# Optimization experiments

Hardware: AMD Instinct MI355X
Metric: run time of the kernel (lower is better)

Reference implementation:

```python
import jax, jax.numpy as jnp
import numpy as np

TAU = 1.0   # temperature
BETA = 1.0  # instance_alingment_weight


def setup_inputs() -> dict:
    key = jax.random.key(0)
    k1, k2, k3 = jax.random.split(key, 3)
    N, D = 1024, 128
    return {
        "x": jax.random.normal(k1, (N, D), dtype=jnp.float32),
        "aug_x": jax.random.normal(k2, (N, D), dtype=jnp.float32),
        "label_prompt_embedding": jax.random.normal(k3, (N, D), dtype=jnp.float32),
    }


def _pair_loss(x, y, scale):
    # positive distances: ||x_i - y_i|| / (tau * sqrt(D)), shape [N]
    pos = jnp.linalg.norm(x - y, axis=1) * scale
    # pairwise distance matrix [N, N] via broadcasted [N, N, D] diff (as original)
    dm = jnp.linalg.norm(x[:, None, :] - y[None, :, :], axis=-1) * scale
    denom = jnp.sum(jnp.exp(dm), axis=1)  # [N]
    # log(exp(pos) / denom) == pos - log(denom)
    return jnp.mean(pos - jnp.log(denom))


def reference(x, aug_x, label_prompt_embedding):
    D = x.shape[-1]
    scale = 1.0 / (TAU * np.sqrt(D).astype(np.float32))
    center_alignment_loss = _pair_loss(x, label_prompt_embedding, scale)
    instance_alignment_loss = _pair_loss(x, aug_x, scale)
    alignment_loss = center_alignment_loss + BETA * instance_alignment_loss
    return (alignment_loss, center_alignment_loss, instance_alignment_loss)
```

## Files before the change

kernel.cpp:

```cpp
#include <hip/hip_runtime.h>
#include <math.h>

#define NN 1024
#define DD 128

typedef __bf16 bf16x8 __attribute__((ext_vector_type(8)));
typedef float  floatx4 __attribute__((ext_vector_type(4)));

__global__ __launch_bounds__(256) void align_pair_kernel(
    const float* __restrict__ x,
    const float* __restrict__ y_center,
    const float* __restrict__ y_aug,
    float* __restrict__ partials )
{
    const float SCALE = 0.08838834764831845f;
    const int p    = blockIdx.y;
    const float* __restrict__ y = p ? y_aug : y_center;
    const int i0   = blockIdx.x * 16;
    const int tid  = threadIdx.x;
    const int w    = tid >> 6;
    const int lane = tid & 63;
    const int col  = lane & 15;
    const int quad = lane >> 4;

    const float* xrow = x + (size_t)(i0 + col) * DD + quad * 8;
    bf16x8 afrag[4];
    float nx_own = 0.f;
#pragma unroll
    for (int c = 0; c < 4; ++c) {
        const float4 u0 = *(const float4*)(xrow + c * 32);
        const float4 u1 = *(const float4*)(xrow + c * 32 + 4);
        nx_own += u0.x*u0.x + u0.y*u0.y + u0.z*u0.z + u0.w*u0.w;
        nx_own += u1.x*u1.x + u1.y*u1.y + u1.z*u1.z + u1.w*u1.w;
        bf16x8 f;
        f[0]=(__bf16)u0.x; f[1]=(__bf16)u0.y; f[2]=(__bf16)u0.z; f[3]=(__bf16)u0.w;
        f[4]=(__bf16)u1.x; f[5]=(__bf16)u1.y; f[6]=(__bf16)u1.z; f[7]=(__bf16)u1.w;
        afrag[c] = f;
    }
    nx_own += __shfl_xor(nx_own, 16);
    nx_own += __shfl_xor(nx_own, 32);
    float nxr[4];
#pragma unroll
    for (int r = 0; r < 4; ++r) nxr[r] = __shfl(nx_own, quad * 4 + r);

    float denom[4] = {0.f, 0.f, 0.f, 0.f};
    float pos[4]   = {0.f, 0.f, 0.f, 0.f};

    for (int t = 0; t < 16; ++t) {
        const int j0 = t * 64 + w * 16;
        const float* yrow = y + (size_t)(j0 + col) * DD + quad * 8;
        bf16x8 bfrag[4];
        float ny_own = 0.f;
#pragma unroll
        for (int c = 0; c < 4; ++c) {
            const float4 u0 = *(const float4*)(yrow + c * 32);
            const float4 u1 = *(const float4*)(yrow + c * 32 + 4);
            ny_own += u0.x*u0.x + u0.y*u0.y + u0.z*u0.z + u0.w*u0.w;
            ny_own += u1.x*u1.x + u1.y*u1.y + u1.z*u1.z + u1.w*u1.w;
            bf16x8 f;
            f[0]=(__bf16)u0.x; f[1]=(__bf16)u0.y; f[2]=(__bf16)u0.z; f[3]=(__bf16)u0.w;
            f[4]=(__bf16)u1.x; f[5]=(__bf16)u1.y; f[6]=(__bf16)u1.z; f[7]=(__bf16)u1.w;
            bfrag[c] = f;
        }
        ny_own += __shfl_xor(ny_own, 16);
        ny_own += __shfl_xor(ny_own, 32);

        floatx4 acc = {0.f, 0.f, 0.f, 0.f};
#pragma unroll
        for (int c = 0; c < 4; ++c)
            acc = __builtin_amdgcn_mfma_f32_16x16x32_bf16(afrag[c], bfrag[c], acc, 0, 0, 0);

#pragma unroll
        for (int r = 0; r < 4; ++r) {
            const int row = quad * 4 + r;
            float d2 = fmaf(-2.f, acc[r], nxr[r] + ny_own);
            d2 = fmaxf(d2, 0.f);
            const float dm = SCALE * sqrtf(d2);
            denom[r] += __expf(dm);
            if (j0 + col == i0 + row) pos[r] = dm;
        }
    }

#pragma unroll
    for (int r = 0; r < 4; ++r) {
#pragma unroll
        for (int m = 1; m < 16; m <<= 1) {
            denom[r] += __shfl_xor(denom[r], m);
            pos[r]   += __shfl_xor(pos[r], m);
        }
    }

    __shared__ float ld_den[4][16];
    __shared__ float ld_pos[4][16];
    if (col == 0) {
#pragma unroll
        for (int r = 0; r < 4; ++r) {
            ld_den[w][quad * 4 + r] = denom[r];
            ld_pos[w][quad * 4 + r] = pos[r];
        }
    }
    __syncthreads();
    __shared__ float ld_c[16];
    if (tid < 16) {
        const float den = ld_den[0][tid] + ld_den[1][tid] + ld_den[2][tid] + ld_den[3][tid];
        const float po  = ld_pos[0][tid] + ld_pos[1][tid] + ld_pos[2][tid] + ld_pos[3][tid];
        ld_c[tid] = po - logf(den);
    }
    __syncthreads();
    if (tid == 0) {
        float s = 0.f;
#pragma unroll
        for (int k = 0; k < 16; ++k) s += ld_c[k];
        partials[p * 64 + blockIdx.x] = s;
    }
}

__global__ void align_finalize(const float* __restrict__ partials, float* __restrict__ out)
{
    const int tid = threadIdx.x;
    float v = partials[tid];
#pragma unroll
    for (int m = 1; m < 64; m <<= 1) v += __shfl_xor(v, m);
    __shared__ float s[2];
    if ((tid & 63) == 0) s[tid >> 6] = v;
    __syncthreads();
    if (tid == 0) {
        const float inv = 1.0f / (float)NN;
        const float c  = s[0] * inv;
        const float ia = s[1] * inv;
        out[0] = c + ia;
        out[1] = c;
        out[2] = ia;
    }
}

extern "C" void kernel_launch(void* const* d_in, const int* in_sizes, int n_in,
                              void* d_out, int out_size, void* d_ws, size_t ws_size,
                              hipStream_t stream) {
    const float* x   = (const float*)d_in[0];
    const float* aug = (const float*)d_in[1];
    const float* lp  = (const float*)d_in[2];
    float* out       = (float*)d_out;
    float* partials  = (float*)d_ws;

    align_pair_kernel<<<dim3(64, 2), 256, 0, stream>>>(x, lp, aug, partials);
    align_finalize<<<1, 128, 0, stream>>>(partials, out);
}
```

Before: 74.02 us.

## Precompute bf16 matrices and norms, split column range across blocks

Adds a prep kernel that converts x, lp and aug to bf16 once and computes their row norms, so the pair kernel no longer reconverts and re-reduces every y tile in every block. The pair kernel's j range is split into 8 chunks across a new grid dimension, which raises the block count from 128 to 1024 to fill the GPU. The partial denominators and positive distances go to workspace and are combined in a 1024-thread finalize kernel. The cost is an extra launch and global round trips for the intermediates.

```diff
diff --git a/kernel.cpp b/kernel.cpp
--- a/kernel.cpp
+++ b/kernel.cpp
@@ -3,67 +3,73 @@
 
 #define NN 1024
 #define DD 128
+#define JCH 8
 
 typedef __bf16 bf16x8 __attribute__((ext_vector_type(8)));
 typedef float  floatx4 __attribute__((ext_vector_type(4)));
 
+#define WS_NORMS  786432
+#define WS_DENOM  798720
+#define WS_POS    864256
+
+__global__ __launch_bounds__(256) void align_prep(
+    const float* __restrict__ x, const float* __restrict__ lp,
+    const float* __restrict__ aug, __bf16* __restrict__ mats,
+    float* __restrict__ norms)
+{
+    const int w    = threadIdx.x >> 6;
+    const int lane = threadIdx.x & 63;
+    const int gw   = blockIdx.x * 4 + w;
+    const int a    = gw >> 10;
+    const int r    = gw & 1023;
+    const float* src = (a == 0 ? x : (a == 1 ? lp : aug)) + (size_t)r * DD + lane * 2;
+    const float2 v = *(const float2*)src;
+    float sq = v.x * v.x + v.y * v.y;
+    union { __bf16 b[2]; unsigned u; } t;
+    t.b[0] = (__bf16)v.x; t.b[1] = (__bf16)v.y;
+    *(unsigned*)(mats + (size_t)a * (NN * DD) + (size_t)r * DD + lane * 2) = t.u;
+#pragma unroll
+    for (int m = 1; m < 64; m <<= 1) sq += __shfl_xor(sq, m);
+    if (lane == 0) norms[a * NN + r] = sq;
+}
+
 __global__ __launch_bounds__(256) void align_pair_kernel(
-    const float* __restrict__ x,
-    const float* __restrict__ y_center,
-    const float* __restrict__ y_aug,
-    float* __restrict__ partials )
+    const __bf16* __restrict__ mats, const float* __restrict__ norms,
+    float* __restrict__ denom_part, float* __restrict__ posbuf)
 {
     const float SCALE = 0.08838834764831845f;
-    const int p    = blockIdx.y;
-    const float* __restrict__ y = p ? y_aug : y_center;
-    const int i0   = blockIdx.x * 16;
+    const int bx = blockIdx.x;
+    const int p  = blockIdx.y;
+    const int jc = blockIdx.z;
+    const __bf16* __restrict__ A = mats;
+    const __bf16* __restrict__ B = mats + (size_t)(p ? 2 : 1) * (NN * DD);
+    const float*  __restrict__ nx = norms;
+    const float*  __restrict__ ny = norms + (p ? 2 : 1) * NN;
+
+    const int i0   = bx * 16;
     const int tid  = threadIdx.x;
     const int w    = tid >> 6;
     const int lane = tid & 63;
     const int col  = lane & 15;
     const int quad = lane >> 4;
 
-    const float* xrow = x + (size_t)(i0 + col) * DD + quad * 8;
+    const __bf16* arow = A + (size_t)(i0 + col) * DD + quad * 8;
     bf16x8 afrag[4];
-    float nx_own = 0.f;
 #pragma unroll
-    for (int c = 0; c < 4; ++c) {
-        const float4 u0 = *(const float4*)(xrow + c * 32);
-        const float4 u1 = *(const float4*)(xrow + c * 32 + 4);
-        nx_own += u0.x*u0.x + u0.y*u0.y + u0.z*u0.z + u0.w*u0.w;
-        nx_own += u1.x*u1.x + u1.y*u1.y + u1.z*u1.z + u1.w*u1.w;
-        bf16x8 f;
-        f[0]=(__bf16)u0.x; f[1]=(__bf16)u0.y; f[2]=(__bf16)u0.z; f[3]=(__bf16)u0.w;
-        f[4]=(__bf16)u1.x; f[5]=(__bf16)u1.y; f[6]=(__bf16)u1.z; f[7]=(__bf16)u1.w;
-        afrag[c] = f;
-    }
-    nx_own += __shfl_xor(nx_own, 16);
-    nx_own += __shfl_xor(nx_own, 32);
-    float nxr[4];
-#pragma unroll
-    for (int r = 0; r < 4; ++r) nxr[r] = __shfl(nx_own, quad * 4 + r);
+    for (int c = 0; c < 4; ++c) afrag[c] = *(const bf16x8*)(arow + c * 32);
+    const float4 nxr = *(const float4*)(nx + i0 + quad * 4);
 
     float denom[4] = {0.f, 0.f, 0.f, 0.f};
     float pos[4]   = {0.f, 0.f, 0.f, 0.f};
 
-    for (int t = 0; t < 16; ++t) {
-        const int j0 = t * 64 + w * 16;
-        const float* yrow = y + (size_t)(j0 + col) * DD + quad * 8;
+#pragma unroll
+    for (int t = 0; t < 2; ++t) {
+        const int j0 = jc * 128 + t * 64 + w * 16;
+        const __bf16* brow = B + (size_t)(j0 + col) * DD + quad * 8;
         bf16x8 bfrag[4];
-        float ny_own = 0.f;
 #pragma unroll
-        for (int c = 0; c < 4; ++c) {
-            const float4 u0 = *(const float4*)(yrow + c * 32);
-            const float4 u1 = *(const float4*)(yrow + c * 32 + 4);
-            ny_own += u0.x*u0.x + u0.y*u0.y + u0.z*u0.z + u0.w*u0.w;
-            ny_own += u1.x*u1.x + u1.y*u1.y + u1.z*u1.z + u1.w*u1.w;
-            bf16x8 f;
-            f[0]=(__bf16)u0.x; f[1]=(__bf16)u0.y; f[2]=(__bf16)u0.z; f[3]=(__bf16)u0.w;
-            f[4]=(__bf16)u1.x; f[5]=(__bf16)u1.y; f[6]=(__bf16)u1.z; f[7]=(__bf16)u1.w;
-            bfrag[c] = f;
-        }
-        ny_own += __shfl_xor(ny_own, 16);
-        ny_own += __shfl_xor(ny_own, 32);
+        for (int c = 0; c < 4; ++c) bfrag[c] = *(const bf16x8*)(brow + c * 32);
+        const float nyv = ny[j0 + col];
 
         floatx4 acc = {0.f, 0.f, 0.f, 0.f};
 #pragma unroll
@@ -73,7 +79,7 @@
 #pragma unroll
         for (int r = 0; r < 4; ++r) {
             const int row = quad * 4 + r;
-            float d2 = fmaf(-2.f, acc[r], nxr[r] + ny_own);
+            float d2 = fmaf(-2.f, acc[r], nxr[r] + nyv);
             d2 = fmaxf(d2, 0.f);
             const float dm = SCALE * sqrtf(d2);
             denom[r] += __expf(dm);
@@ -100,34 +106,48 @@
         }
     }
     __syncthreads();
-    __shared__ float ld_c[16];
     if (tid < 16) {
         const float den = ld_den[0][tid] + ld_den[1][tid] + ld_den[2][tid] + ld_den[3][tid];
-        const float po  = ld_pos[0][tid] + ld_pos[1][tid] + ld_pos[2][tid] + ld_pos[3][tid];
-        ld_c[tid] = po - logf(den);
-    }
-    __syncthreads();
-    if (tid == 0) {
-        float s = 0.f;
-#pragma unroll
-        for (int k = 0; k < 16; ++k) s += ld_c[k];
-        partials[p * 64 + blockIdx.x] = s;
+        denom_part[(size_t)(p * JCH + jc) * NN + i0 + tid] = den;
+        if (jc == (bx >> 3)) {
+            const float po = ld_pos[0][tid] + ld_pos[1][tid] + ld_pos[2][tid] + ld_pos[3][tid];
+            posbuf[p * NN + i0 + tid] = po;
+        }
     }
 }
 
-__global__ void align_finalize(const float* __restrict__ partials, float* __restrict__ out)
+__global__ __launch_bounds__(1024) void align_finalize(
+    const float* __restrict__ denom_part, const float* __restrict__ posbuf,
+    float* __restrict__ out)
 {
-    const int tid = threadIdx.x;
-    float v = partials[tid];
+    const int tid  = threadIdx.x;
+    const int w    = tid >> 6;
+    const int lane = tid & 63;
+    float contrib[2];
 #pragma unroll
-    for (int m = 1; m < 64; m <<= 1) v += __shfl_xor(v, m);
-    __shared__ float s[2];
-    if ((tid & 63) == 0) s[tid >> 6] = v;
+    for (int p = 0; p < 2; ++p) {
+        float den = 0.f;
+#pragma unroll
+        for (int jc = 0; jc < JCH; ++jc)
+            den += denom_part[(size_t)(p * JCH + jc) * NN + tid];
+        contrib[p] = posbuf[p * NN + tid] - __logf(den);
+    }
+    float c0 = contrib[0], c1 = contrib[1];
+#pragma unroll
+    for (int m = 1; m < 64; m <<= 1) {
+        c0 += __shfl_xor(c0, m);
+        c1 += __shfl_xor(c1, m);
+    }
+    __shared__ float s0[16], s1[16];
+    if (lane == 0) { s0[w] = c0; s1[w] = c1; }
     __syncthreads();
     if (tid == 0) {
+        float a = 0.f, b = 0.f;
+#pragma unroll
+        for (int k = 0; k < 16; ++k) { a += s0[k]; b += s1[k]; }
         const float inv = 1.0f / (float)NN;
-        const float c  = s[0] * inv;
-        const float ia = s[1] * inv;
+        const float c  = a * inv;
+        const float ia = b * inv;
         out[0] = c + ia;
         out[1] = c;
         out[2] = ia;
@@ -141,8 +161,14 @@
     const float* aug = (const float*)d_in[1];
     const float* lp  = (const float*)d_in[2];
     float* out       = (float*)d_out;
-    float* partials  = (float*)d_ws;
 
-    align_pair_kernel<<<dim3(64, 2), 256, 0, stream>>>(x, lp, aug, partials);
-    align_finalize<<<1, 128, 0, stream>>>(partials, out);
+    char* ws = (char*)d_ws;
+    __bf16* mats      = (__bf16*)ws;
+    float*  norms     = (float*)(ws + WS_NORMS);
+    float*  denom_par = (float*)(ws + WS_DENOM);
+    float*  posbuf    = (float*)(ws + WS_POS);
+
+    align_prep<<<768, 256, 0, stream>>>(x, lp, aug, mats, norms);
+    align_pair_kernel<<<dim3(64, 2, JCH), 256, 0, stream>>>(mats, norms, denom_par, posbuf);
+    align_finalize<<<1, 1024, 0, stream>>>(denom_par, posbuf, out);
 }
```

Measured after the change: 67.69 us. 1.09x faster.
